# Kernel optimization log

Hardware: AMD Instinct MI355X
Metric: run time of the kernel (lower is better)

## Reference

```python
import jax, jax.numpy as jnp
import numpy as np

N_NODES = 100000
N_EDGES = 1600000
D = 128


def setup_inputs() -> dict:
    key = jax.random.key(0)
    k1, k2, k3, k4, k5 = jax.random.split(key, 5)
    features = jax.random.normal(k1, (N_NODES, D), dtype=jnp.float32)
    edge_src = jax.random.randint(k2, (N_EDGES,), 0, N_NODES, dtype=jnp.int32)
    edge_dst = jax.random.randint(k3, (N_EDGES,), 0, N_NODES, dtype=jnp.int32)
    edge_vals = jax.random.uniform(k4, (N_EDGES,), dtype=jnp.float32)
    # Glorot uniform for W (in_dim == out_dim == D), zeros bias
    limit = float(np.sqrt(6.0 / (D + D)))
    W = jax.random.uniform(k5, (D, D), dtype=jnp.float32, minval=-limit, maxval=limit)
    b = jnp.zeros((D,), dtype=jnp.float32)
    return {"features": features, "edge_src": edge_src, "edge_dst": edge_dst,
            "edge_vals": edge_vals, "W": W, "b": b}


def reference(features, edge_src, edge_dst, edge_vals, W, b):
    # support = features @ W  : [N, D]
    support = features @ W
    # sparse adjacency SpMM: out[d] = sum_e vals[e] * support[src[e]] for dst[e]==d
    msgs = support[edge_src] * edge_vals[:, None]          # [E, D]
    out = jax.ops.segment_sum(msgs, edge_dst, num_segments=N_NODES)  # [N, D]
    out = jax.nn.relu(out + b)
    # residual (in_dim == out_dim)
    return out + features
```

## Files before the change

kernel.cpp:

```cpp
#include <hip/hip_runtime.h>
#include <hip/hip_bf16.h>

#define NN 100000
#define NE 1600000
#define D 128
#define NB 196
#define BSH 9
#define CAP 10240

static constexpr int NA    = (NE + 4095) / 4096;
static constexpr int NGEMM = (NN + 63) / 64;

static constexpr size_t SUP_OFF    = 0;
static constexpr size_t SUP_BYTES  = (((size_t)NN * D * 2) + 15) & ~(size_t)15;
static constexpr size_t RB_OFF     = SUP_OFF + SUP_BYTES;
static constexpr size_t RB_BY      = (((size_t)NN * 4) + 15) & ~(size_t)15;
static constexpr size_t RE_OFF     = RB_OFF + RB_BY;
static constexpr size_t RE_BY      = (((size_t)NN * 4) + 15) & ~(size_t)15;
static constexpr size_t CUR_OFF    = RE_OFF + RE_BY;
static constexpr size_t CUR_BY     = (((size_t)NB * 4) + 15) & ~(size_t)15;
static constexpr size_t WT_OFF     = CUR_OFF + CUR_BY;
static constexpr size_t WT_BY      = (size_t)D * D * 2;
static constexpr size_t STG_OFF    = WT_OFF + WT_BY;
static constexpr size_t STG_BY     = (size_t)NB * CAP * 8;
static constexpr size_t EDG_OFF    = STG_OFF + STG_BY;
static constexpr size_t EDG_BY     = (size_t)NB * CAP * 4;

typedef __attribute__((ext_vector_type(8))) short short8v;
typedef __attribute__((ext_vector_type(4))) float float4v;
typedef __attribute__((ext_vector_type(4))) unsigned uint4v;

__device__ __forceinline__ unsigned pk_bf16(float a, float b) {
  __hip_bfloat16 x = __float2bfloat16(a), y = __float2bfloat16(b);
  return (unsigned)*(unsigned short*)&x | ((unsigned)*(unsigned short*)&y << 16);
}

__global__ __launch_bounds__(256) void k0_prep(const float* __restrict__ W,
                                               unsigned short* __restrict__ Wt,
                                               int* __restrict__ cursor) {
  const int i = blockIdx.x * 256 + threadIdx.x;
  if (i < D * D) {
    const int k = i >> 7, c = i & 127;
    __hip_bfloat16 h = __float2bfloat16(W[i]);
    Wt[c * D + k] = *(unsigned short*)&h;
  }
  if (blockIdx.x == 0 && threadIdx.x < NB) cursor[threadIdx.x] = 0;
}

__global__ __launch_bounds__(256) void kpassA(const int* __restrict__ src,
                                              const int* __restrict__ dst,
                                              const float* __restrict__ val,
                                              int* __restrict__ cursor,
                                              unsigned long long* __restrict__ stg) {
  __shared__ int h4[4 * NB];
  __shared__ int h[NB];
  __shared__ int base[NB];
  const int t = threadIdx.x;
  for (int i = t; i < 4 * NB; i += 256) h4[i] = 0;
  __syncthreads();
  const int e0 = blockIdx.x * 4096;
  const int hb = (t >> 6) * NB;
  int d[16];
#pragma unroll
  for (int k = 0; k < 16; ++k) {
    const int e = e0 + t + k * 256;
    d[k] = (e < NE) ? dst[e] : -1;
    if (d[k] >= 0) atomicAdd(&h4[hb + (d[k] >> BSH)], 1);
  }
  __syncthreads();
  for (int i = t; i < NB; i += 256)
    h[i] = h4[i] + h4[NB + i] + h4[2 * NB + i] + h4[3 * NB + i];
  __syncthreads();
  for (int i = t; i < NB; i += 256)
    base[i] = h[i] ? atomicAdd(&cursor[i], h[i]) : 0;
  __syncthreads();
#pragma unroll
  for (int k = 0; k < 16; ++k) {
    const int e = e0 + t + k * 256;
    if (d[k] >= 0) {
      const int bk = d[k] >> BSH;
      const int pos = atomicAdd(&base[bk], 1);
      const unsigned lo = (unsigned)src[e] | ((unsigned)(d[k] & 511) << 17);
      const unsigned hi = __float_as_uint(val[e]);
      stg[(size_t)bk * CAP + pos] = (unsigned long long)lo | ((unsigned long long)hi << 32);
    }
  }
}

__global__ __launch_bounds__(256) void k2_passB_gemm(const unsigned long long* __restrict__ stg,
                                                     const int* __restrict__ cursor,
                                                     int* __restrict__ rowBeg,
                                                     int* __restrict__ rowEnd,
                                                     unsigned* __restrict__ edges,
                                                     const float* __restrict__ feat,
                                                     const unsigned short* __restrict__ Wt,
                                                     unsigned short* __restrict__ sup) {
  const int t = threadIdx.x;
  if ((int)blockIdx.x < NB) {
    __shared__ int hist[512];
    __shared__ int start[512];
    __shared__ int psum[256];
    const int b = blockIdx.x;
    const int cnt = cursor[b];
    const int base = b * CAP;
    hist[t] = 0;
    hist[t + 256] = 0;
    __syncthreads();
    for (int i = t; i < cnt; i += 256)
      atomicAdd(&hist[((unsigned)stg[base + i] >> 17) & 511], 1);
    __syncthreads();
    const int h0 = hist[2 * t], h1 = hist[2 * t + 1];
    const int p = h0 + h1;
    psum[t] = p;
    __syncthreads();
#pragma unroll
    for (int off = 1; off < 256; off <<= 1) {
      const int x = (t >= off) ? psum[t - off] : 0;
      __syncthreads();
      psum[t] += x;
      __syncthreads();
    }
    const int ex = psum[t] - p;
    start[2 * t] = ex;
    start[2 * t + 1] = ex + h0;
    __syncthreads();
    const int node0 = b << BSH;
    for (int j = t; j < 512; j += 256) {
      const int node = node0 + j;
      if (node < NN) {
        rowBeg[node] = base + start[j];
        rowEnd[node] = base + start[j] + hist[j];
      }
    }
    __syncthreads();
    for (int j = t; j < 512; j += 256) hist[j] = start[j];
    __syncthreads();
    for (int i = t; i < cnt; i += 256) {
      const unsigned long long pk = stg[base + i];
      const unsigned lo = (unsigned)pk;
      const int dl = (lo >> 17) & 511;
      const int pos = base + atomicAdd(&hist[dl], 1);
      __hip_bfloat16 hv = __float2bfloat16(__uint_as_float((unsigned)(pk >> 32)));
      edges[pos] = (lo & 0x1FFFFu) | ((unsigned)*(unsigned short*)&hv << 17);
    }
  } else {
    const int gid = (int)blockIdx.x - NB;
    __shared__ char Wl[32768];
    {
      const uint4* g = (const uint4*)Wt;
      for (int i = t; i < 2048; i += 256) {
        const int b = i << 4;
        *(uint4*)&Wl[b ^ (((b >> 8) & 7) << 4)] = g[i];
      }
    }
    __syncthreads();

    const int wv = t >> 6, l = t & 63;
    const int lm = l & 15, lk = l >> 4;
    const int r0 = gid * 64 + wv * 16;
    int row = r0 + lm;
    if (row >= NN) row = NN - 1;
    const float* fr = feat + (size_t)row * D;

    short8v A[4];
#pragma unroll
    for (int ks = 0; ks < 4; ++ks) {
      const float4 u = *(const float4*)(fr + ks * 32 + lk * 8);
      const float4 v = *(const float4*)(fr + ks * 32 + lk * 8 + 4);
      union { unsigned w[4]; short8v s; } cv;
      cv.w[0] = pk_bf16(u.x, u.y);
      cv.w[1] = pk_bf16(u.z, u.w);
      cv.w[2] = pk_bf16(v.x, v.y);
      cv.w[3] = pk_bf16(v.z, v.w);
      A[ks] = cv.s;
    }

    float4v acc[8];
#pragma unroll
    for (int ct = 0; ct < 8; ++ct) acc[ct] = (float4v){0.f, 0.f, 0.f, 0.f};

#pragma unroll
    for (int ct = 0; ct < 8; ++ct) {
      const int c = ct * 16 + lm;
#pragma unroll
      for (int ks = 0; ks < 4; ++ks) {
        int b = c * 256 + ks * 64 + lk * 16;
        b ^= ((c & 7) << 4);
        const short8v Bf = *(const short8v*)&Wl[b];
        acc[ct] = __builtin_amdgcn_mfma_f32_16x16x32_bf16(A[ks], Bf, acc[ct], 0, 0, 0);
      }
    }

#pragma unroll
    for (int j = 0; j < 4; ++j) {
      const int rr = r0 + lk * 4 + j;
      if (rr < NN) {
        unsigned short* srow = sup + (size_t)rr * D + lm;
#pragma unroll
        for (int ct = 0; ct < 8; ++ct) {
          __hip_bfloat16 h = __float2bfloat16(acc[ct][j]);
          srow[ct * 16] = *(unsigned short*)&h;
        }
      }
    }
  }
}

__global__ __launch_bounds__(256) void kgather(const unsigned short* __restrict__ sup,
                                               const int* __restrict__ rowBeg,
                                               const int* __restrict__ rowEnd,
                                               const unsigned* __restrict__ edges,
                                               const float* __restrict__ feat,
                                               const float* __restrict__ bias,
                                               float* __restrict__ out) {
  const int n = blockIdx.x * 16 + (threadIdx.x >> 4);
  if (n >= NN) return;
  const int gl = threadIdx.x & 15;
  const int beg = rowBeg[n];
  const int end = rowEnd[n];
  float a0 = 0.f, a1 = 0.f, a2 = 0.f, a3 = 0.f, a4 = 0.f, a5 = 0.f, a6 = 0.f, a7 = 0.f;

  const char* supb = (const char*)sup;
  const unsigned glo = (unsigned)(gl << 4);

#define ACC8(q, rr)                                                        \
  {                                                                        \
    const float vv = __uint_as_float((rr >> 17) << 16);                    \
    a0 = fmaf(__uint_as_float(q.x << 16), vv, a0);                         \
    a1 = fmaf(__uint_as_float(q.x & 0xffff0000u), vv, a1);                 \
    a2 = fmaf(__uint_as_float(q.y << 16), vv, a2);                         \
    a3 = fmaf(__uint_as_float(q.y & 0xffff0000u), vv, a3);                 \
    a4 = fmaf(__uint_as_float(q.z << 16), vv, a4);                         \
    a5 = fmaf(__uint_as_float(q.z & 0xffff0000u), vv, a5);                 \
    a6 = fmaf(__uint_as_float(q.w << 16), vv, a6);                         \
    a7 = fmaf(__uint_as_float(q.w & 0xffff0000u), vv, a7);                 \
  }

  unsigned w = 0;
  if (beg + gl < end) w = __builtin_nontemporal_load(edges + beg + gl);

  for (int base = beg; base < end; base += 16) {
    int cnt = end - base;
    if (cnt > 16) cnt = 16;
    const unsigned wc = w;
    if (base + 16 + gl < end) w = __builtin_nontemporal_load(edges + base + 16 + gl);

    int i = 0;
    for (; i + 8 <= cnt; i += 8) {
      const unsigned r0 = __shfl(wc, i + 0, 16);
      const unsigned r1 = __shfl(wc, i + 1, 16);
      const unsigned r2 = __shfl(wc, i + 2, 16);
      const unsigned r3 = __shfl(wc, i + 3, 16);
      const unsigned r4 = __shfl(wc, i + 4, 16);
      const unsigned r5 = __shfl(wc, i + 5, 16);
      const unsigned r6 = __shfl(wc, i + 6, 16);
      const unsigned r7 = __shfl(wc, i + 7, 16);
      const uint4v q0 = *(const uint4v*)(supb + ((r0 & 0x1FFFFu) << 8) + glo);
      const uint4v q1 = *(const uint4v*)(supb + ((r1 & 0x1FFFFu) << 8) + glo);
      const uint4v q2 = *(const uint4v*)(supb + ((r2 & 0x1FFFFu) << 8) + glo);
      const uint4v q3 = *(const uint4v*)(supb + ((r3 & 0x1FFFFu) << 8) + glo);
      const uint4v q4 = *(const uint4v*)(supb + ((r4 & 0x1FFFFu) << 8) + glo);
      const uint4v q5 = *(const uint4v*)(supb + ((r5 & 0x1FFFFu) << 8) + glo);
      const uint4v q6 = *(const uint4v*)(supb + ((r6 & 0x1FFFFu) << 8) + glo);
      const uint4v q7 = *(const uint4v*)(supb + ((r7 & 0x1FFFFu) << 8) + glo);
      ACC8(q0, r0) ACC8(q1, r1) ACC8(q2, r2) ACC8(q3, r3)
      ACC8(q4, r4) ACC8(q5, r5) ACC8(q6, r6) ACC8(q7, r7)
    }
    for (; i < cnt; ++i) {
      const unsigned rr = __shfl(wc, i, 16);
      const uint4v q = *(const uint4v*)(supb + ((rr & 0x1FFFFu) << 8) + glo);
      ACC8(q, rr)
    }
  }
#undef ACC8

  const int c = gl << 3;
  const float4v b0 = *(const float4v*)(bias + c);
  const float4v b1 = *(const float4v*)(bias + c + 4);
  const float* frt = feat + (size_t)n * D + c;
  const float4v f0 = __builtin_nontemporal_load((const float4v*)frt);
  const float4v f1 = __builtin_nontemporal_load((const float4v*)(frt + 4));
  float4v o0, o1;
  o0.x = fmaxf(a0 + b0.x, 0.f) + f0.x;
  o0.y = fmaxf(a1 + b0.y, 0.f) + f0.y;
  o0.z = fmaxf(a2 + b0.z, 0.f) + f0.z;
  o0.w = fmaxf(a3 + b0.w, 0.f) + f0.w;
  o1.x = fmaxf(a4 + b1.x, 0.f) + f1.x;
  o1.y = fmaxf(a5 + b1.y, 0.f) + f1.y;
  o1.z = fmaxf(a6 + b1.z, 0.f) + f1.z;
  o1.w = fmaxf(a7 + b1.w, 0.f) + f1.w;
  float* orow = out + (size_t)n * D + c;
  __builtin_nontemporal_store(o0, (float4v*)orow);
  __builtin_nontemporal_store(o1, (float4v*)(orow + 4));
}

extern "C" void kernel_launch(void* const* d_in, const int* in_sizes, int n_in,
                              void* d_out, int out_size, void* d_ws, size_t ws_size,
                              hipStream_t stream) {
  const float* feat = (const float*)d_in[0];
  const int*   esrc = (const int*)d_in[1];
  const int*   edst = (const int*)d_in[2];
  const float* eval = (const float*)d_in[3];
  const float* W    = (const float*)d_in[4];
  const float* bias = (const float*)d_in[5];
  float* out = (float*)d_out;
  char*  ws  = (char*)d_ws;

  unsigned short*     sup    = (unsigned short*)(ws + SUP_OFF);
  int*                rowBeg = (int*)(ws + RB_OFF);
  int*                rowEnd = (int*)(ws + RE_OFF);
  int*                cursor = (int*)(ws + CUR_OFF);
  unsigned short*     Wt     = (unsigned short*)(ws + WT_OFF);
  unsigned long long* stg    = (unsigned long long*)(ws + STG_OFF);
  unsigned*           edges  = (unsigned*)(ws + EDG_OFF);

  k0_prep<<<64, 256, 0, stream>>>(W, Wt, cursor);
  kpassA<<<NA, 256, 0, stream>>>(esrc, edst, eval, cursor, stg);
  k2_passB_gemm<<<NB + NGEMM, 256, 0, stream>>>(stg, cursor, rowBeg, rowEnd, edges,
                                                feat, Wt, sup);
  kgather<<<(NN + 15) / 16, 256, 0, stream>>>(sup, rowBeg, rowEnd, edges, feat, bias, out);
}
```

Measured before the change: 131.3 us.

## Split feature GEMM across pass-A and pass-B kernels to balance load

Moves the dense feature×W GEMM tiles into a shared device function and runs about half of the tiles alongside the edge-bucketing pass A, with the other half staying alongside pass B. Pass A also drops its four per-wave histogram copies in favour of a single shared-memory histogram, and both kernels reuse one shared LDS buffer. The goal is to fill idle compute units during the short, atomic-bound pass A and shorten pass B. The cost is higher LDS use for pass-A blocks, which may reduce occupancy, and more contention on the single histogram.

Result: faster. 128.1 us (median of 2 runs) (-2.4%).

```diff
diff --git a/kernel.cpp b/kernel.cpp
--- a/kernel.cpp
+++ b/kernel.cpp
@@ -10,6 +10,8 @@
 
 static constexpr int NA    = (NE + 4095) / 4096;
 static constexpr int NGEMM = (NN + 63) / 64;
+static constexpr int GH1   = 781;
+static constexpr int GH2   = NGEMM - GH1;
 
 static constexpr size_t SUP_OFF    = 0;
 static constexpr size_t SUP_BYTES  = (((size_t)NN * D * 2) + 15) & ~(size_t)15;
@@ -47,43 +49,110 @@
   if (blockIdx.x == 0 && threadIdx.x < NB) cursor[threadIdx.x] = 0;
 }
 
-__global__ __launch_bounds__(256) void kpassA(const int* __restrict__ src,
-                                              const int* __restrict__ dst,
-                                              const float* __restrict__ val,
-                                              int* __restrict__ cursor,
-                                              unsigned long long* __restrict__ stg) {
-  __shared__ int h4[4 * NB];
-  __shared__ int h[NB];
-  __shared__ int base[NB];
+__device__ __forceinline__ void gemm_tile(const int gid, const int t,
+                                          const float* __restrict__ feat,
+                                          const unsigned short* __restrict__ Wt,
+                                          unsigned short* __restrict__ sup,
+                                          char* Wl) {
+  {
+    const uint4* g = (const uint4*)Wt;
+    for (int i = t; i < 2048; i += 256) {
+      const int b = i << 4;
+      *(uint4*)&Wl[b ^ (((b >> 8) & 7) << 4)] = g[i];
+    }
+  }
+  __syncthreads();
+
+  const int wv = t >> 6, l = t & 63;
+  const int lm = l & 15, lk = l >> 4;
+  const int r0 = gid * 64 + wv * 16;
+  int row = r0 + lm;
+  if (row >= NN) row = NN - 1;
+  const float* fr = feat + (size_t)row * D;
+
+  short8v A[4];
+#pragma unroll
+  for (int ks = 0; ks < 4; ++ks) {
+    const float4 u = *(const float4*)(fr + ks * 32 + lk * 8);
+    const float4 v = *(const float4*)(fr + ks * 32 + lk * 8 + 4);
+    union { unsigned w[4]; short8v s; } cv;
+    cv.w[0] = pk_bf16(u.x, u.y);
+    cv.w[1] = pk_bf16(u.z, u.w);
+    cv.w[2] = pk_bf16(v.x, v.y);
+    cv.w[3] = pk_bf16(v.z, v.w);
+    A[ks] = cv.s;
+  }
+
+  float4v acc[8];
+#pragma unroll
+  for (int ct = 0; ct < 8; ++ct) acc[ct] = (float4v){0.f, 0.f, 0.f, 0.f};
+
+#pragma unroll
+  for (int ct = 0; ct < 8; ++ct) {
+    const int c = ct * 16 + lm;
+#pragma unroll
+    for (int ks = 0; ks < 4; ++ks) {
+      int b = c * 256 + ks * 64 + lk * 16;
+      b ^= ((c & 7) << 4);
+      const short8v Bf = *(const short8v*)&Wl[b];
+      acc[ct] = __builtin_amdgcn_mfma_f32_16x16x32_bf16(A[ks], Bf, acc[ct], 0, 0, 0);
+    }
+  }
+
+#pragma unroll
+  for (int j = 0; j < 4; ++j) {
+    const int rr = r0 + lk * 4 + j;
+    if (rr < NN) {
+      unsigned short* srow = sup + (size_t)rr * D + lm;
+#pragma unroll
+      for (int ct = 0; ct < 8; ++ct) {
+        __hip_bfloat16 h = __float2bfloat16(acc[ct][j]);
+        srow[ct * 16] = *(unsigned short*)&h;
+      }
+    }
+  }
+}
+
+__global__ __launch_bounds__(256) void k1_passA_gemm(const int* __restrict__ src,
+                                                     const int* __restrict__ dst,
+                                                     const float* __restrict__ val,
+                                                     int* __restrict__ cursor,
+                                                     unsigned long long* __restrict__ stg,
+                                                     const float* __restrict__ feat,
+                                                     const unsigned short* __restrict__ Wt,
+                                                     unsigned short* __restrict__ sup) {
+  __shared__ char ldsbuf[32768];
   const int t = threadIdx.x;
-  for (int i = t; i < 4 * NB; i += 256) h4[i] = 0;
-  __syncthreads();
-  const int e0 = blockIdx.x * 4096;
-  const int hb = (t >> 6) * NB;
-  int d[16];
-#pragma unroll
-  for (int k = 0; k < 16; ++k) {
-    const int e = e0 + t + k * 256;
-    d[k] = (e < NE) ? dst[e] : -1;
-    if (d[k] >= 0) atomicAdd(&h4[hb + (d[k] >> BSH)], 1);
-  }
-  __syncthreads();
-  for (int i = t; i < NB; i += 256)
-    h[i] = h4[i] + h4[NB + i] + h4[2 * NB + i] + h4[3 * NB + i];
-  __syncthreads();
-  for (int i = t; i < NB; i += 256)
-    base[i] = h[i] ? atomicAdd(&cursor[i], h[i]) : 0;
-  __syncthreads();
-#pragma unroll
-  for (int k = 0; k < 16; ++k) {
-    const int e = e0 + t + k * 256;
-    if (d[k] >= 0) {
-      const int bk = d[k] >> BSH;
-      const int pos = atomicAdd(&base[bk], 1);
-      const unsigned lo = (unsigned)src[e] | ((unsigned)(d[k] & 511) << 17);
-      const unsigned hi = __float_as_uint(val[e]);
-      stg[(size_t)bk * CAP + pos] = (unsigned long long)lo | ((unsigned long long)hi << 32);
-    }
+  if ((int)blockIdx.x < NA) {
+    int* h    = (int*)ldsbuf;
+    int* base = ((int*)ldsbuf) + NB;
+    for (int i = t; i < NB; i += 256) h[i] = 0;
+    __syncthreads();
+    const int e0 = blockIdx.x * 4096;
+    int d[16];
+#pragma unroll
+    for (int k = 0; k < 16; ++k) {
+      const int e = e0 + t + k * 256;
+      d[k] = (e < NE) ? dst[e] : -1;
+      if (d[k] >= 0) atomicAdd(&h[d[k] >> BSH], 1);
+    }
+    __syncthreads();
+    for (int i = t; i < NB; i += 256)
+      base[i] = h[i] ? atomicAdd(&cursor[i], h[i]) : 0;
+    __syncthreads();
+#pragma unroll
+    for (int k = 0; k < 16; ++k) {
+      const int e = e0 + t + k * 256;
+      if (d[k] >= 0) {
+        const int bk = d[k] >> BSH;
+        const int pos = atomicAdd(&base[bk], 1);
+        const unsigned lo = (unsigned)src[e] | ((unsigned)(d[k] & 511) << 17);
+        const unsigned hi = __float_as_uint(val[e]);
+        stg[(size_t)bk * CAP + pos] = (unsigned long long)lo | ((unsigned long long)hi << 32);
+      }
+    }
+  } else {
+    gemm_tile((int)blockIdx.x - NA, t, feat, Wt, sup, ldsbuf);
   }
 }
 
@@ -95,11 +164,12 @@
                                                      const float* __restrict__ feat,
                                                      const unsigned short* __restrict__ Wt,
                                                      unsigned short* __restrict__ sup) {
+  __shared__ char ldsbuf[32768];
   const int t = threadIdx.x;
   if ((int)blockIdx.x < NB) {
-    __shared__ int hist[512];
-    __shared__ int start[512];
-    __shared__ int psum[256];
+    int* hist  = (int*)ldsbuf;
+    int* start = ((int*)ldsbuf) + 512;
+    int* psum  = ((int*)ldsbuf) + 1024;
     const int b = blockIdx.x;
     const int cnt = cursor[b];
     const int base = b * CAP;
@@ -144,65 +214,7 @@
       edges[pos] = (lo & 0x1FFFFu) | ((unsigned)*(unsigned short*)&hv << 17);
     }
   } else {
-    const int gid = (int)blockIdx.x - NB;
-    __shared__ char Wl[32768];
-    {
-      const uint4* g = (const uint4*)Wt;
-      for (int i = t; i < 2048; i += 256) {
-        const int b = i << 4;
-        *(uint4*)&Wl[b ^ (((b >> 8) & 7) << 4)] = g[i];
-      }
-    }
-    __syncthreads();
-
-    const int wv = t >> 6, l = t & 63;
-    const int lm = l & 15, lk = l >> 4;
-    const int r0 = gid * 64 + wv * 16;
-    int row = r0 + lm;
-    if (row >= NN) row = NN - 1;
-    const float* fr = feat + (size_t)row * D;
-
-    short8v A[4];
-#pragma unroll
-    for (int ks = 0; ks < 4; ++ks) {
-      const float4 u = *(const float4*)(fr + ks * 32 + lk * 8);
-      const float4 v = *(const float4*)(fr + ks * 32 + lk * 8 + 4);
-      union { unsigned w[4]; short8v s; } cv;
-      cv.w[0] = pk_bf16(u.x, u.y);
-      cv.w[1] = pk_bf16(u.z, u.w);
-      cv.w[2] = pk_bf16(v.x, v.y);
-      cv.w[3] = pk_bf16(v.z, v.w);
-      A[ks] = cv.s;
-    }
-
-    float4v acc[8];
-#pragma unroll
-    for (int ct = 0; ct < 8; ++ct) acc[ct] = (float4v){0.f, 0.f, 0.f, 0.f};
-
-#pragma unroll
-    for (int ct = 0; ct < 8; ++ct) {
-      const int c = ct * 16 + lm;
-#pragma unroll
-      for (int ks = 0; ks < 4; ++ks) {
-        int b = c * 256 + ks * 64 + lk * 16;
-        b ^= ((c & 7) << 4);
-        const short8v Bf = *(const short8v*)&Wl[b];
-        acc[ct] = __builtin_amdgcn_mfma_f32_16x16x32_bf16(A[ks], Bf, acc[ct], 0, 0, 0);
-      }
-    }
-
-#pragma unroll
-    for (int j = 0; j < 4; ++j) {
-      const int rr = r0 + lk * 4 + j;
-      if (rr < NN) {
-        unsigned short* srow = sup + (size_t)rr * D + lm;
-#pragma unroll
-        for (int ct = 0; ct < 8; ++ct) {
-          __hip_bfloat16 h = __float2bfloat16(acc[ct][j]);
-          srow[ct * 16] = *(unsigned short*)&h;
-        }
-      }
-    }
+    gemm_tile((int)blockIdx.x - NB + GH1, t, feat, Wt, sup, ldsbuf);
   }
 }
 
@@ -315,8 +327,8 @@
   unsigned*           edges  = (unsigned*)(ws + EDG_OFF);
 
   k0_prep<<<64, 256, 0, stream>>>(W, Wt, cursor);
-  kpassA<<<NA, 256, 0, stream>>>(esrc, edst, eval, cursor, stg);
-  k2_passB_gemm<<<NB + NGEMM, 256, 0, stream>>>(stg, cursor, rowBeg, rowEnd, edges,
-                                                feat, Wt, sup);
+  k1_passA_gemm<<<NA + GH1, 256, 0, stream>>>(esrc, edst, eval, cursor, stg, feat, Wt, sup);
+  k2_passB_gemm<<<NB + GH2, 256, 0, stream>>>(stg, cursor, rowBeg, rowEnd, edges,
+                                              feat, Wt, sup);
   kgather<<<(NN + 15) / 16, 256, 0, stream>>>(sup, rowBeg, rowEnd, edges, feat, bias, out);
 }
```
